# Performance work log

Hardware: AMD Instinct MI355X
Metric: run time of the kernel (lower is better)

Reference implementation:

```python
import jax, jax.numpy as jnp
import numpy as np

B, C, H, W = 8, 128, 64, 64

def setup_inputs() -> dict:
    key = jax.random.key(0)
    ks = jax.random.split(key, 8)
    s = 1.0 / np.sqrt(C)
    return {
        "x": jax.random.normal(ks[0], (B, C, H, W), dtype=jnp.float32),
        "dw_q": jax.random.normal(ks[1], (C,), dtype=jnp.float32) * s,
        "pw_q": jax.random.normal(ks[2], (C, C), dtype=jnp.float32) * s,
        "dw_k": jax.random.normal(ks[3], (C,), dtype=jnp.float32) * s,
        "pw_k": jax.random.normal(ks[4], (C, C), dtype=jnp.float32) * s,
        "dw_v": jax.random.normal(ks[5], (C,), dtype=jnp.float32) * s,
        "pw_v": jax.random.normal(ks[6], (C, C), dtype=jnp.float32) * s,
        "gamma": jnp.zeros((1,), dtype=jnp.float32) + 0.5,
    }

def _proj(x, dw, pw):
    # depthwise 1x1 (groups=C, no bias) == per-channel scale; then pointwise 1x1 conv (C_out=C)
    xs = x * dw[None, :, None, None]
    return jnp.einsum('oc,bchw->bohw', pw, xs)

def reference(x, dw_q, pw_q, dw_k, pw_k, dw_v, pw_v, gamma):
    b, c, h, w = x.shape
    n = h * w
    q = _proj(x, dw_q, pw_q).reshape(b, c, n)   # B,C,N
    k = _proj(x, dw_k, pw_k).reshape(b, c, n)
    v = _proj(x, dw_v, pw_v).reshape(b, c, n)
    # energy[b,n,m] = sum_c q[b,c,n] k[b,c,m]  (no scaling, as in source)
    energy = jnp.einsum('bcn,bcm->bnm', q, k)
    attn = jax.nn.softmax(energy, axis=-1)      # B,N,N
    # out[b,c,n] = sum_m v[b,c,m] attn[b,n,m]
    out = jnp.einsum('bcm,bnm->bcn', v, attn).reshape(b, c, h, w)
    return gamma[0] * out + x
```

## Files before the change

### kernel.cpp

```cpp
#include <hip/hip_runtime.h>
#include <hip/hip_bf16.h>


typedef __bf16 v8bf __attribute__((ext_vector_type(8)));
typedef float  v4f  __attribute__((ext_vector_type(4)));

#define B_ 8
#define C_ 128
#define N_ 4096

#define SWZ(R, COLS) ((R) * 160 + (((((COLS) >> 3) ^ (((R) >> 2) & 15))) << 3) + ((COLS) & 7))

static __device__ __forceinline__ unsigned short f2bf_rne(float f) {
    union { float f; unsigned u; } v; v.f = f;
    return (unsigned short)((v.u + 0x7fffu + ((v.u >> 16) & 1u)) >> 16);
}
static __device__ __forceinline__ unsigned fbits(float f) {
    union { float f; unsigned u; } v; v.f = f; return v.u;
}

__global__ __launch_bounds__(256, 2) void proj_kernel(
    const float* __restrict__ x,
    const float* __restrict__ dw_q, const float* __restrict__ pw_q,
    const float* __restrict__ dw_k, const float* __restrict__ pw_k,
    const float* __restrict__ dw_v, const float* __restrict__ pw_v,
    unsigned short* __restrict__ qf_ws, unsigned short* __restrict__ kt,
    unsigned short* __restrict__ vt)
{
    __shared__ unsigned short xT[128 * 160];
    __shared__ unsigned short Ws[128 * 160];

    const int bid = blockIdx.x;
    const int bb  = bid & 7;
    const int t   = (bid >> 3) & 31;
    const int pp  = bid >> 8;
    const int n0  = t * 128;
    const int tid = threadIdx.x;
    const int w    = tid >> 6;
    const int lane = tid & 63;
    const int quad = lane >> 4;
    const int l16  = lane & 15;

    #pragma unroll
    for (int k = 0; k < 16; ++k) {
        const int idx = tid + k * 256;
        const int c  = idx >> 5;
        const int nq = idx & 31;
        float4 f = *(const float4*)(x + ((size_t)(bb * C_ + c)) * N_ + n0 + nq * 4);
        xT[SWZ(nq * 4 + 0, c)] = f2bf_rne(f.x);
        xT[SWZ(nq * 4 + 1, c)] = f2bf_rne(f.y);
        xT[SWZ(nq * 4 + 2, c)] = f2bf_rne(f.z);
        xT[SWZ(nq * 4 + 3, c)] = f2bf_rne(f.w);
    }
    const float* pw = (pp == 0) ? pw_q : (pp == 1) ? pw_k : pw_v;
    const float* dw = (pp == 0) ? dw_q : (pp == 1) ? dw_k : dw_v;
    const float qs = (pp == 0) ? 1.4426950408889634f : 1.0f;
    #pragma unroll
    for (int k = 0; k < 16; ++k) {
        const int idx = tid + k * 256;
        const int o  = idx >> 5;
        const int c4 = (idx & 31) * 4;
        float4 p4 = *(const float4*)(pw + o * 128 + c4);
        float4 d4 = *(const float4*)(dw + c4);
        unsigned lo = (unsigned)f2bf_rne(p4.x * d4.x * qs) | ((unsigned)f2bf_rne(p4.y * d4.y * qs) << 16);
        unsigned hi = (unsigned)f2bf_rne(p4.z * d4.z * qs) | ((unsigned)f2bf_rne(p4.w * d4.w * qs) << 16);
        *(unsigned long long*)&Ws[SWZ(o, c4)] =
            (unsigned long long)lo | ((unsigned long long)hi << 32);
    }
    __syncthreads();

    const unsigned short* As = (pp < 2) ? xT : Ws;
    const unsigned short* Bs = (pp < 2) ? Ws : xT;

    v4f acc[2][8];
    #pragma unroll
    for (int i = 0; i < 2; ++i)
        #pragma unroll
        for (int j = 0; j < 8; ++j)
            acc[i][j] = (v4f){0.f, 0.f, 0.f, 0.f};

    #pragma unroll
    for (int kc = 0; kc < 4; ++kc) {
        v8bf av[2];
        #pragma unroll
        for (int i = 0; i < 2; ++i)
            av[i] = *(const v8bf*)&As[SWZ(w * 32 + i * 16 + l16, kc * 32 + quad * 8)];
        #pragma unroll
        for (int cb = 0; cb < 8; ++cb) {
            v8bf bv = *(const v8bf*)&Bs[SWZ(cb * 16 + l16, kc * 32 + quad * 8)];
            acc[0][cb] = __builtin_amdgcn_mfma_f32_16x16x32_bf16(av[0], bv, acc[0][cb], 0, 0, 0);
            acc[1][cb] = __builtin_amdgcn_mfma_f32_16x16x32_bf16(av[1], bv, acc[1][cb], 0, 0, 0);
        }
    }
    __syncthreads();

    unsigned short* sc = Ws;
    #pragma unroll
    for (int mi = 0; mi < 2; ++mi)
        #pragma unroll
        for (int cb = 0; cb < 8; ++cb)
            #pragma unroll
            for (int r = 0; r < 4; ++r)
                sc[SWZ(w * 32 + mi * 16 + quad * 4 + r, cb * 16 + l16)] =
                    f2bf_rne(acc[mi][cb][r]);
    __syncthreads();

    if (pp == 0) {
        unsigned short* dst = qf_ws + ((size_t)(bb * 64 + t * 2)) * 8192;
        #pragma unroll
        for (int p = 0; p < 8; ++p) {
            const int g     = p * 4 + w;
            const int strip = g >> 4, ni = (g >> 2) & 3, kc = g & 3;
            *(uint4*)(dst + ((size_t)g * 64 + lane) * 8) =
                *(const uint4*)&sc[SWZ(strip * 64 + ni * 16 + l16, kc * 32 + quad * 8)];
        }
    } else if (pp == 1) {
        unsigned short* dst = kt + ((size_t)(bb * 32 + t)) * 16384;
        #pragma unroll
        for (int p = 0; p < 8; ++p) {
            const int g  = p * 4 + w;
            const int mb = g >> 2, kc = g & 3;
            *(uint4*)(dst + ((size_t)g * 64 + lane) * 8) =
                *(const uint4*)&sc[SWZ(mb * 16 + l16, kc * 32 + quad * 8)];
        }
    } else {
        unsigned short* dst = vt + ((size_t)(bb * 32 + t)) * 16384;
        #pragma unroll
        for (int p = 0; p < 8; ++p) {
            const int d  = p * 256 + tid;
            const int cb = d >> 8, wq = (d >> 4) & 15, l = d & 15;
            *(uint4*)(dst + (size_t)d * 8) =
                *(const uint4*)&sc[SWZ(cb * 16 + l, wq * 8)];
        }
    }
}

#define MFMA(A, B, C) __builtin_amdgcn_mfma_f32_16x16x32_bf16(A, B, C, 0, 0, 0)
#define EXP2(X) __builtin_amdgcn_exp2f(X)
#define PKPERM(EH, EL) __builtin_amdgcn_perm(fbits(EH), fbits(EL), 0x07060302)

#define LOADK(KF, TILE) { \
    const unsigned short* kp_ = kbase + (size_t)(TILE) * 16384; \
    _Pragma("unroll") \
    for (int mi_ = 0; mi_ < 2; ++mi_) \
        _Pragma("unroll") \
        for (int kc_ = 0; kc_ < 4; ++kc_) \
            KF[mi_][kc_] = *(const v8bf*)(kp_ + (size_t)((mi_ * 4 + kc_) * 64) * 8); \
}

#define LOADV(TILE) { \
    const unsigned short* vp_ = vbase + (size_t)(TILE) * 16384; \
    _Pragma("unroll") \
    for (int cb_ = 0; cb_ < 8; ++cb_) \
        vf[cb_] = *(const v8bf*)(vp_ + (size_t)(cb_ * 256) * 8); \
}

#define MKPF(NI, PK0A, PK0B, PK1A, PK1B) { \
    unsigned sLo_ = (quad < 2) ? PK0A : PK1A; \
    unsigned sHi_ = (quad < 2) ? PK0B : PK1B; \
    union { unsigned u[4]; v8bf v; } pu_; \
    pu_.u[0] = (unsigned)__builtin_amdgcn_ds_bpermute(la, (int)sLo_); \
    pu_.u[1] = (unsigned)__builtin_amdgcn_ds_bpermute(la, (int)sHi_); \
    pu_.u[2] = (unsigned)__builtin_amdgcn_ds_bpermute(lb, (int)sLo_); \
    pu_.u[3] = (unsigned)__builtin_amdgcn_ds_bpermute(lb, (int)sHi_); \
    pf[NI] = pu_.v; \
}

#define SCOMP0(KF, SC) { \
    _Pragma("unroll") \
    for (int mi_ = 0; mi_ < 2; ++mi_) \
        _Pragma("unroll") \
        for (int ni_ = 0; ni_ < 2; ++ni_) { \
            v4f a_ = MFMA(KF[mi_][0], qf[ni_][0], Z4v); \
            _Pragma("unroll") \
            for (int kc_ = 1; kc_ < 4; ++kc_) \
                a_ = MFMA(KF[mi_][kc_], qf[ni_][kc_], a_); \
            SC[mi_][ni_] = a_; \
        } \
}

#define FUSED(SC_IN, KF, SC_OUT) { \
    float e0_, e1_, e2_, e3_; \
    unsigned pk00a_, pk00b_, pk10a_, pk10b_, pk01a_, pk01b_, pk11a_, pk11b_; \
    SC_OUT[0][0] = MFMA(KF[0][0], qf[0][0], Z4v); \
    SC_OUT[0][1] = MFMA(KF[0][0], qf[1][0], Z4v); \
    e0_ = EXP2(SC_IN[0][0][0]); e1_ = EXP2(SC_IN[0][0][1]); \
    e2_ = EXP2(SC_IN[0][0][2]); e3_ = EXP2(SC_IN[0][0][3]); \
    SC_OUT[0][0] = MFMA(KF[0][1], qf[0][1], SC_OUT[0][0]); \
    SC_OUT[0][1] = MFMA(KF[0][1], qf[1][1], SC_OUT[0][1]); \
    lpart[0] += (e0_ + e1_) + (e2_ + e3_); \
    pk00a_ = PKPERM(e1_, e0_); pk00b_ = PKPERM(e3_, e2_); \
    SC_OUT[0][0] = MFMA(KF[0][2], qf[0][2], SC_OUT[0][0]); \
    SC_OUT[0][1] = MFMA(KF[0][2], qf[1][2], SC_OUT[0][1]); \
    e0_ = EXP2(SC_IN[1][0][0]); e1_ = EXP2(SC_IN[1][0][1]); \
    e2_ = EXP2(SC_IN[1][0][2]); e3_ = EXP2(SC_IN[1][0][3]); \
    SC_OUT[0][0] = MFMA(KF[0][3], qf[0][3], SC_OUT[0][0]); \
    SC_OUT[0][1] = MFMA(KF[0][3], qf[1][3], SC_OUT[0][1]); \
    lpart[0] += (e0_ + e1_) + (e2_ + e3_); \
    pk10a_ = PKPERM(e1_, e0_); pk10b_ = PKPERM(e3_, e2_); \
    SC_OUT[1][0] = MFMA(KF[1][0], qf[0][0], Z4v); \
    SC_OUT[1][1] = MFMA(KF[1][0], qf[1][0], Z4v); \
    MKPF(0, pk00a_, pk00b_, pk10a_, pk10b_) \
    SC_OUT[1][0] = MFMA(KF[1][1], qf[0][1], SC_OUT[1][0]); \
    SC_OUT[1][1] = MFMA(KF[1][1], qf[1][1], SC_OUT[1][1]); \
    e0_ = EXP2(SC_IN[0][1][0]); e1_ = EXP2(SC_IN[0][1][1]); \
    e2_ = EXP2(SC_IN[0][1][2]); e3_ = EXP2(SC_IN[0][1][3]); \
    SC_OUT[1][0] = MFMA(KF[1][2], qf[0][2], SC_OUT[1][0]); \
    SC_OUT[1][1] = MFMA(KF[1][2], qf[1][2], SC_OUT[1][1]); \
    lpart[1] += (e0_ + e1_) + (e2_ + e3_); \
    pk01a_ = PKPERM(e1_, e0_); pk01b_ = PKPERM(e3_, e2_); \
    SC_OUT[1][0] = MFMA(KF[1][3], qf[0][3], SC_OUT[1][0]); \
    SC_OUT[1][1] = MFMA(KF[1][3], qf[1][3], SC_OUT[1][1]); \
    e0_ = EXP2(SC_IN[1][1][0]); e1_ = EXP2(SC_IN[1][1][1]); \
    e2_ = EXP2(SC_IN[1][1][2]); e3_ = EXP2(SC_IN[1][1][3]); \
    lpart[1] += (e0_ + e1_) + (e2_ + e3_); \
    pk11a_ = PKPERM(e1_, e0_); pk11b_ = PKPERM(e3_, e2_); \
    MKPF(1, pk01a_, pk01b_, pk11a_, pk11b_) \
}

#define PVOP { \
    _Pragma("unroll") \
    for (int ni_ = 0; ni_ < 2; ++ni_) \
        _Pragma("unroll") \
        for (int cb_ = 0; cb_ < 8; ++cb_) \
            oacc[cb_][ni_] = MFMA(vf[cb_], pf[ni_], oacc[cb_][ni_]); \
}

__global__ __launch_bounds__(256, 2) void attn_kernel(
    const unsigned short* __restrict__ qf_ws, const unsigned short* __restrict__ kt,
    const unsigned short* __restrict__ vt, const float* __restrict__ x,
    const float* __restrict__ gamma, float* __restrict__ out)
{
    __shared__ float red[32 * 132];
    __shared__ float l_s[4][32];

    const int bid = blockIdx.x;
    const int bb  = bid & 7;
    const int s   = bid >> 3;
    const int n0  = s * 32;
    const int tid = threadIdx.x;
    const int w    = tid >> 6;
    const int lane = tid & 63;
    const int quad = lane >> 4;
    const int l16  = lane & 15;

    v8bf qf[2][4];
    {
        const unsigned short* qb = qf_ws + ((size_t)(bb * 128 + s)) * 4096;
        #pragma unroll
        for (int ni = 0; ni < 2; ++ni)
            #pragma unroll
            for (int kc = 0; kc < 4; ++kc)
                qf[ni][kc] = *(const v8bf*)(qb + ((size_t)(ni * 4 + kc) * 64 + lane) * 8);
    }

    v4f oacc[8][2];
    #pragma unroll
    for (int i = 0; i < 8; ++i)
        #pragma unroll
        for (int j = 0; j < 2; ++j)
            oacc[i][j] = (v4f){0.f, 0.f, 0.f, 0.f};
    float lpart[2] = {0.f, 0.f};
    const v4f Z4v = {0.f, 0.f, 0.f, 0.f};

    const int la = ((((quad & 1) << 1) << 4) + l16) << 2;
    const int lb = la + 64;

    const unsigned short* kbase = kt + ((size_t)(bb * 32)) * 16384 + ((size_t)(w * 8) * 64 + lane) * 8;
    const unsigned short* vbase = vt + ((size_t)(bb * 32)) * 16384 + ((size_t)(w * 64 + lane)) * 8;

    v8bf kfA[2][4], kfB[2][4], vf[8];
    v4f sc0[2][2], sc1[2][2];
    v8bf pf[2];

    LOADK(kfA, 0)
    LOADV(0)
    LOADK(kfB, 1)
    SCOMP0(kfA, sc0)

    for (int it = 0; it < 32; it += 2) {
        LOADK(kfA, (it + 2) & 31)
        FUSED(sc0, kfB, sc1)
        PVOP
        LOADV((it + 1) & 31)
        LOADK(kfB, (it + 3) & 31)
        FUSED(sc1, kfA, sc0)
        PVOP
        LOADV((it + 2) & 31)
    }

    #pragma unroll
    for (int ni = 0; ni < 2; ++ni) {
        float r = lpart[ni];
        r += __shfl_xor(r, 16);
        r += __shfl_xor(r, 32);
        if (lane < 16) l_s[w][ni * 16 + lane] = r;
    }

    for (int rw = 0; rw < 4; ++rw) {
        if (w == rw) {
            #pragma unroll
            for (int cb = 0; cb < 8; ++cb)
                #pragma unroll
                for (int ni = 0; ni < 2; ++ni) {
                    float* p = &red[(ni * 16 + l16) * 132 + cb * 16 + quad * 4];
                    if (rw == 0) *(v4f*)p = oacc[cb][ni];
                    else {
                        v4f tv = *(const v4f*)p;
                        tv += oacc[cb][ni];
                        *(v4f*)p = tv;
                    }
                }
        }
        __syncthreads();
    }

    const float g = gamma[0];
    const int   n = tid & 31;
    const int  cg = tid >> 5;
    const float li = 1.0f / (((l_s[0][n] + l_s[1][n]) + (l_s[2][n] + l_s[3][n])));
    #pragma unroll
    for (int j = 0; j < 16; ++j) {
        const int c = cg * 16 + j;
        const size_t idx = ((size_t)(bb * C_ + c)) * N_ + n0 + n;
        out[idx] = g * red[n * 132 + c] * li + x[idx];
    }
}

extern "C" void kernel_launch(void* const* d_in, const int* in_sizes, int n_in,
                              void* d_out, int out_size, void* d_ws, size_t ws_size,
                              hipStream_t stream)
{
    (void)in_sizes; (void)n_in; (void)out_size; (void)ws_size;
    const float* x     = (const float*)d_in[0];
    const float* dw_q  = (const float*)d_in[1];
    const float* pw_q  = (const float*)d_in[2];
    const float* dw_k  = (const float*)d_in[3];
    const float* pw_k  = (const float*)d_in[4];
    const float* dw_v  = (const float*)d_in[5];
    const float* pw_v  = (const float*)d_in[6];
    const float* gamma = (const float*)d_in[7];
    float* out = (float*)d_out;

    unsigned short* qf_ws = (unsigned short*)d_ws;
    unsigned short* kt    = qf_ws + (size_t)B_ * N_ * C_;
    unsigned short* vt    = kt    + (size_t)B_ * N_ * C_;

    proj_kernel<<<dim3(768), dim3(256), 0, stream>>>(
        x, dw_q, pw_q, dw_k, pw_k, dw_v, pw_v, qf_ws, kt, vt);
    attn_kernel<<<dim3(1024), dim3(256), 0, stream>>>(
        qf_ws, kt, vt, x, gamma, out);
}
```

Measured before the change: 174.1 us.

## Switch attention Q/K/V and probabilities to FP8 MFMA

Projection outputs Q, K and V are now packed to FP8 (e4m3) in a new fragment layout, and the attention kernel uses 16x16x32 fp8 MFMA for both QK^T and PV. Softmax probabilities are packed to FP8 with cvt_pk_fp8, which halves the ds_bpermute traffic. The aim is to halve workspace bandwidth and register footprint and to use higher-throughput FP8 matrix ops. In exchange, the much lower precision of the scores and probabilities (no scaling is applied) risks accuracy failures, especially since the unscaled energies feed exp2.

```diff
diff --git a/kernel.cpp b/kernel.cpp
--- a/kernel.cpp
+++ b/kernel.cpp
@@ -4,6 +4,7 @@
 
 typedef __bf16 v8bf __attribute__((ext_vector_type(8)));
 typedef float  v4f  __attribute__((ext_vector_type(4)));
+typedef unsigned long long u64;
 
 #define B_ 8
 #define C_ 128
@@ -15,8 +16,19 @@
     union { float f; unsigned u; } v; v.f = f;
     return (unsigned short)((v.u + 0x7fffu + ((v.u >> 16) & 1u)) >> 16);
 }
-static __device__ __forceinline__ unsigned fbits(float f) {
-    union { float f; unsigned u; } v; v.f = f; return v.u;
+
+static __device__ __forceinline__ u64 bf8pack(uint4 s) {
+    float f[8];
+    #pragma unroll
+    for (int j = 0; j < 8; ++j) {
+        unsigned hs = (j & 1) ? ((&s.x)[j >> 1] >> 16) : ((&s.x)[j >> 1] & 0xffffu);
+        union { unsigned u; float f; } t; t.u = hs << 16; f[j] = t.f;
+    }
+    int lo = __builtin_amdgcn_cvt_pk_fp8_f32(f[0], f[1], 0, false);
+    lo     = __builtin_amdgcn_cvt_pk_fp8_f32(f[2], f[3], lo, true);
+    int hi = __builtin_amdgcn_cvt_pk_fp8_f32(f[4], f[5], 0, false);
+    hi     = __builtin_amdgcn_cvt_pk_fp8_f32(f[6], f[7], hi, true);
+    return (u64)(unsigned)lo | ((u64)(unsigned)hi << 32);
 }
 
 __global__ __launch_bounds__(256, 2) void proj_kernel(
@@ -24,8 +36,8 @@
     const float* __restrict__ dw_q, const float* __restrict__ pw_q,
     const float* __restrict__ dw_k, const float* __restrict__ pw_k,
     const float* __restrict__ dw_v, const float* __restrict__ pw_v,
-    unsigned short* __restrict__ qf_ws, unsigned short* __restrict__ kt,
-    unsigned short* __restrict__ vt)
+    unsigned char* __restrict__ qf8, unsigned char* __restrict__ kt8,
+    unsigned char* __restrict__ vt8)
 {
     __shared__ unsigned short xT[128 * 160];
     __shared__ unsigned short Ws[128 * 160];
@@ -106,64 +118,80 @@
     __syncthreads();
 
     if (pp == 0) {
-        unsigned short* dst = qf_ws + ((size_t)(bb * 64 + t * 2)) * 8192;
+        unsigned char* dst = qf8 + (size_t)bb * 524288;
         #pragma unroll
         for (int p = 0; p < 8; ++p) {
             const int g     = p * 4 + w;
             const int strip = g >> 4, ni = (g >> 2) & 3, kc = g & 3;
-            *(uint4*)(dst + ((size_t)g * 64 + lane) * 8) =
-                *(const uint4*)&sc[SWZ(strip * 64 + ni * 16 + l16, kc * 32 + quad * 8)];
+            uint4 sv = *(const uint4*)&sc[SWZ(strip * 64 + ni * 16 + l16, kc * 32 + quad * 8)];
+            *(u64*)(dst + (size_t)(t * 4 + strip * 2 + (ni >> 1)) * 4096
+                        + ((ni & 1) * 2 + (kc >> 1)) * 1024 + lane * 16 + (kc & 1) * 8)
+                = bf8pack(sv);
         }
     } else if (pp == 1) {
-        unsigned short* dst = kt + ((size_t)(bb * 32 + t)) * 16384;
+        unsigned char* dst = kt8 + (size_t)(bb * 32 + t) * 16384;
         #pragma unroll
         for (int p = 0; p < 8; ++p) {
             const int g  = p * 4 + w;
             const int mb = g >> 2, kc = g & 3;
-            *(uint4*)(dst + ((size_t)g * 64 + lane) * 8) =
-                *(const uint4*)&sc[SWZ(mb * 16 + l16, kc * 32 + quad * 8)];
+            uint4 sv = *(const uint4*)&sc[SWZ(mb * 16 + l16, kc * 32 + quad * 8)];
+            *(u64*)(dst + (mb * 2 + (kc >> 1)) * 1024 + lane * 16 + (kc & 1) * 8)
+                = bf8pack(sv);
         }
     } else {
-        unsigned short* dst = vt + ((size_t)(bb * 32 + t)) * 16384;
+        unsigned char* dst = vt8 + (size_t)(bb * 32 + t) * 16384;
         #pragma unroll
         for (int p = 0; p < 8; ++p) {
-            const int d  = p * 256 + tid;
-            const int cb = d >> 8, wq = (d >> 4) & 15, l = d & 15;
-            *(uint4*)(dst + (size_t)d * 8) =
-                *(const uint4*)&sc[SWZ(cb * 16 + l, wq * 8)];
-        }
-    }
-}
-
-#define MFMA(A, B, C) __builtin_amdgcn_mfma_f32_16x16x32_bf16(A, B, C, 0, 0, 0)
+            const int d   = p * 256 + tid;
+            const int cb  = d >> 8;
+            const int wqm = (d >> 6) & 3;
+            const int q16 = (d >> 4) & 15;
+            const int l   = d & 15;
+            const int lnS = d & 63;
+            uint4 sv = *(const uint4*)&sc[SWZ(cb * 16 + l, q16 * 8)];
+            *(u64*)(dst + ((cb >> 1) * 4 + wqm) * 1024 + lnS * 16 + (cb & 1) * 8)
+                = bf8pack(sv);
+        }
+    }
+}
+
+#define MFMA8(A, B, C) __builtin_amdgcn_mfma_f32_16x16x32_fp8_fp8((long)(A), (long)(B), C, 0, 0, 0)
 #define EXP2(X) __builtin_amdgcn_exp2f(X)
-#define PKPERM(EH, EL) __builtin_amdgcn_perm(fbits(EH), fbits(EL), 0x07060302)
+#define PK8(E0, E1, E2, E3, W) { \
+    W = __builtin_amdgcn_cvt_pk_fp8_f32(E0, E1, 0, false); \
+    W = __builtin_amdgcn_cvt_pk_fp8_f32(E2, E3, W, true); \
+}
+
+#define SPLIT16(U4, LO, HI) { \
+    LO = (u64)(U4).x | ((u64)(U4).y << 32); \
+    HI = (u64)(U4).z | ((u64)(U4).w << 32); \
+}
 
 #define LOADK(KF, TILE) { \
-    const unsigned short* kp_ = kbase + (size_t)(TILE) * 16384; \
+    const unsigned char* kp_ = kbase + (size_t)(TILE) * 16384; \
     _Pragma("unroll") \
     for (int mi_ = 0; mi_ < 2; ++mi_) \
         _Pragma("unroll") \
-        for (int kc_ = 0; kc_ < 4; ++kc_) \
-            KF[mi_][kc_] = *(const v8bf*)(kp_ + (size_t)((mi_ * 4 + kc_) * 64) * 8); \
+        for (int kcp_ = 0; kcp_ < 2; ++kcp_) { \
+            uint4 u_ = *(const uint4*)(kp_ + (mi_ * 2 + kcp_) * 1024); \
+            SPLIT16(u_, KF[mi_][kcp_ * 2], KF[mi_][kcp_ * 2 + 1]) \
+        } \
 }
 
 #define LOADV(TILE) { \
-    const unsigned short* vp_ = vbase + (size_t)(TILE) * 16384; \
+    const unsigned char* vp_ = vbase + (size_t)(TILE) * 16384; \
     _Pragma("unroll") \
-    for (int cb_ = 0; cb_ < 8; ++cb_) \
-        vf[cb_] = *(const v8bf*)(vp_ + (size_t)(cb_ * 256) * 8); \
-}
-
-#define MKPF(NI, PK0A, PK0B, PK1A, PK1B) { \
-    unsigned sLo_ = (quad < 2) ? PK0A : PK1A; \
-    unsigned sHi_ = (quad < 2) ? PK0B : PK1B; \
-    union { unsigned u[4]; v8bf v; } pu_; \
-    pu_.u[0] = (unsigned)__builtin_amdgcn_ds_bpermute(la, (int)sLo_); \
-    pu_.u[1] = (unsigned)__builtin_amdgcn_ds_bpermute(la, (int)sHi_); \
-    pu_.u[2] = (unsigned)__builtin_amdgcn_ds_bpermute(lb, (int)sLo_); \
-    pu_.u[3] = (unsigned)__builtin_amdgcn_ds_bpermute(lb, (int)sHi_); \
-    pf[NI] = pu_.v; \
+    for (int cbp_ = 0; cbp_ < 4; ++cbp_) { \
+        uint4 u_ = *(const uint4*)(vp_ + cbp_ * 4096); \
+        SPLIT16(u_, vf[cbp_ * 2], vf[cbp_ * 2 + 1]) \
+    } \
+}
+
+#define MKPF8(NI, PK0, PK1) { \
+    int s_ = (quad < 2) ? PK0 : PK1; \
+    u64 lo_ = (unsigned)__builtin_amdgcn_ds_bpermute(la, s_); \
+    u64 hi_ = (unsigned)__builtin_amdgcn_ds_bpermute(lb, s_); \
+    pf[NI] = lo_ | (hi_ << 32); \
 }
 
 #define SCOMP0(KF, SC) { \
@@ -171,51 +199,51 @@
     for (int mi_ = 0; mi_ < 2; ++mi_) \
         _Pragma("unroll") \
         for (int ni_ = 0; ni_ < 2; ++ni_) { \
-            v4f a_ = MFMA(KF[mi_][0], qf[ni_][0], Z4v); \
+            v4f a_ = MFMA8(KF[mi_][0], qf[ni_][0], Z4v); \
             _Pragma("unroll") \
             for (int kc_ = 1; kc_ < 4; ++kc_) \
-                a_ = MFMA(KF[mi_][kc_], qf[ni_][kc_], a_); \
+                a_ = MFMA8(KF[mi_][kc_], qf[ni_][kc_], a_); \
             SC[mi_][ni_] = a_; \
         } \
 }
 
 #define FUSED(SC_IN, KF, SC_OUT) { \
     float e0_, e1_, e2_, e3_; \
-    unsigned pk00a_, pk00b_, pk10a_, pk10b_, pk01a_, pk01b_, pk11a_, pk11b_; \
-    SC_OUT[0][0] = MFMA(KF[0][0], qf[0][0], Z4v); \
-    SC_OUT[0][1] = MFMA(KF[0][0], qf[1][0], Z4v); \
+    int pk00_, pk10_, pk01_, pk11_; \
+    SC_OUT[0][0] = MFMA8(KF[0][0], qf[0][0], Z4v); \
+    SC_OUT[0][1] = MFMA8(KF[0][0], qf[1][0], Z4v); \
     e0_ = EXP2(SC_IN[0][0][0]); e1_ = EXP2(SC_IN[0][0][1]); \
     e2_ = EXP2(SC_IN[0][0][2]); e3_ = EXP2(SC_IN[0][0][3]); \
-    SC_OUT[0][0] = MFMA(KF[0][1], qf[0][1], SC_OUT[0][0]); \
-    SC_OUT[0][1] = MFMA(KF[0][1], qf[1][1], SC_OUT[0][1]); \
+    SC_OUT[0][0] = MFMA8(KF[0][1], qf[0][1], SC_OUT[0][0]); \
+    SC_OUT[0][1] = MFMA8(KF[0][1], qf[1][1], SC_OUT[0][1]); \
     lpart[0] += (e0_ + e1_) + (e2_ + e3_); \
-    pk00a_ = PKPERM(e1_, e0_); pk00b_ = PKPERM(e3_, e2_); \
-    SC_OUT[0][0] = MFMA(KF[0][2], qf[0][2], SC_OUT[0][0]); \
-    SC_OUT[0][1] = MFMA(KF[0][2], qf[1][2], SC_OUT[0][1]); \
+    PK8(e0_, e1_, e2_, e3_, pk00_) \
+    SC_OUT[0][0] = MFMA8(KF[0][2], qf[0][2], SC_OUT[0][0]); \
+    SC_OUT[0][1] = MFMA8(KF[0][2], qf[1][2], SC_OUT[0][1]); \
     e0_ = EXP2(SC_IN[1][0][0]); e1_ = EXP2(SC_IN[1][0][1]); \
     e2_ = EXP2(SC_IN[1][0][2]); e3_ = EXP2(SC_IN[1][0][3]); \
-    SC_OUT[0][0] = MFMA(KF[0][3], qf[0][3], SC_OUT[0][0]); \
-    SC_OUT[0][1] = MFMA(KF[0][3], qf[1][3], SC_OUT[0][1]); \
+    SC_OUT[0][0] = MFMA8(KF[0][3], qf[0][3], SC_OUT[0][0]); \
+    SC_OUT[0][1] = MFMA8(KF[0][3], qf[1][3], SC_OUT[0][1]); \
     lpart[0] += (e0_ + e1_) + (e2_ + e3_); \
-    pk10a_ = PKPERM(e1_, e0_); pk10b_ = PKPERM(e3_, e2_); \
-    SC_OUT[1][0] = MFMA(KF[1][0], qf[0][0], Z4v); \
-    SC_OUT[1][1] = MFMA(KF[1][0], qf[1][0], Z4v); \
-    MKPF(0, pk00a_, pk00b_, pk10a_, pk10b_) \
-    SC_OUT[1][0] = MFMA(KF[1][1], qf[0][1], SC_OUT[1][0]); \
-    SC_OUT[1][1] = MFMA(KF[1][1], qf[1][1], SC_OUT[1][1]); \
+    PK8(e0_, e1_, e2_, e3_, pk10_) \
+    SC_OUT[1][0] = MFMA8(KF[1][0], qf[0][0], Z4v); \
+    SC_OUT[1][1] = MFMA8(KF[1][0], qf[1][0], Z4v); \
+    MKPF8(0, pk00_, pk10_) \
+    SC_OUT[1][0] = MFMA8(KF[1][1], qf[0][1], SC_OUT[1][0]); \
+    SC_OUT[1][1] = MFMA8(KF[1][1], qf[1][1], SC_OUT[1][1]); \
     e0_ = EXP2(SC_IN[0][1][0]); e1_ = EXP2(SC_IN[0][1][1]); \
     e2_ = EXP2(SC_IN[0][1][2]); e3_ = EXP2(SC_IN[0][1][3]); \
-    SC_OUT[1][0] = MFMA(KF[1][2], qf[0][2], SC_OUT[1][0]); \
-    SC_OUT[1][1] = MFMA(KF[1][2], qf[1][2], SC_OUT[1][1]); \
+    SC_OUT[1][0] = MFMA8(KF[1][2], qf[0][2], SC_OUT[1][0]); \
+    SC_OUT[1][1] = MFMA8(KF[1][2], qf[1][2], SC_OUT[1][1]); \
     lpart[1] += (e0_ + e1_) + (e2_ + e3_); \
-    pk01a_ = PKPERM(e1_, e0_); pk01b_ = PKPERM(e3_, e2_); \
-    SC_OUT[1][0] = MFMA(KF[1][3], qf[0][3], SC_OUT[1][0]); \
-    SC_OUT[1][1] = MFMA(KF[1][3], qf[1][3], SC_OUT[1][1]); \
+    PK8(e0_, e1_, e2_, e3_, pk01_) \
+    SC_OUT[1][0] = MFMA8(KF[1][3], qf[0][3], SC_OUT[1][0]); \
+    SC_OUT[1][1] = MFMA8(KF[1][3], qf[1][3], SC_OUT[1][1]); \
     e0_ = EXP2(SC_IN[1][1][0]); e1_ = EXP2(SC_IN[1][1][1]); \
     e2_ = EXP2(SC_IN[1][1][2]); e3_ = EXP2(SC_IN[1][1][3]); \
     lpart[1] += (e0_ + e1_) + (e2_ + e3_); \
-    pk11a_ = PKPERM(e1_, e0_); pk11b_ = PKPERM(e3_, e2_); \
-    MKPF(1, pk01a_, pk01b_, pk11a_, pk11b_) \
+    PK8(e0_, e1_, e2_, e3_, pk11_) \
+    MKPF8(1, pk01_, pk11_) \
 }
 
 #define PVOP { \
@@ -223,12 +251,12 @@
     for (int ni_ = 0; ni_ < 2; ++ni_) \
         _Pragma("unroll") \
         for (int cb_ = 0; cb_ < 8; ++cb_) \
-            oacc[cb_][ni_] = MFMA(vf[cb_], pf[ni_], oacc[cb_][ni_]); \
+            oacc[cb_][ni_] = MFMA8(vf[cb_], pf[ni_], oacc[cb_][ni_]); \
 }
 
 __global__ __launch_bounds__(256, 2) void attn_kernel(
-    const unsigned short* __restrict__ qf_ws, const unsigned short* __restrict__ kt,
-    const unsigned short* __restrict__ vt, const float* __restrict__ x,
+    const unsigned char* __restrict__ qf8, const unsigned char* __restrict__ kt8,
+    const unsigned char* __restrict__ vt8, const float* __restrict__ x,
     const float* __restrict__ gamma, float* __restrict__ out)
 {
     __shared__ float red[32 * 132];
@@ -244,14 +272,16 @@
     const int quad = lane >> 4;
     const int l16  = lane & 15;
 
-    v8bf qf[2][4];
+    u64 qf[2][4];
     {
-        const unsigned short* qb = qf_ws + ((size_t)(bb * 128 + s)) * 4096;
+        const unsigned char* qb = qf8 + (size_t)(bb * 128 + s) * 4096 + lane * 16;
         #pragma unroll
         for (int ni = 0; ni < 2; ++ni)
             #pragma unroll
-            for (int kc = 0; kc < 4; ++kc)
-                qf[ni][kc] = *(const v8bf*)(qb + ((size_t)(ni * 4 + kc) * 64 + lane) * 8);
+            for (int kcp = 0; kcp < 2; ++kcp) {
+                uint4 u = *(const uint4*)(qb + (ni * 2 + kcp) * 1024);
+                SPLIT16(u, qf[ni][kcp * 2], qf[ni][kcp * 2 + 1])
+            }
     }
 
     v4f oacc[8][2];
@@ -266,12 +296,11 @@
     const int la = ((((quad & 1) << 1) << 4) + l16) << 2;
     const int lb = la + 64;
 
-    const unsigned short* kbase = kt + ((size_t)(bb * 32)) * 16384 + ((size_t)(w * 8) * 64 + lane) * 8;
-    const unsigned short* vbase = vt + ((size_t)(bb * 32)) * 16384 + ((size_t)(w * 64 + lane)) * 8;
-
-    v8bf kfA[2][4], kfB[2][4], vf[8];
+    const unsigned char* kbase = kt8 + (size_t)(bb * 32) * 16384 + w * 4096 + lane * 16;
+    const unsigned char* vbase = vt8 + (size_t)(bb * 32) * 16384 + w * 1024 + lane * 16;
+
+    u64 kfA[2][4], kfB[2][4], vf[8], pf[2];
     v4f sc0[2][2], sc1[2][2];
-    v8bf pf[2];
 
     LOADK(kfA, 0)
     LOADV(0)
@@ -342,12 +371,12 @@
     const float* gamma = (const float*)d_in[7];
     float* out = (float*)d_out;
 
-    unsigned short* qf_ws = (unsigned short*)d_ws;
-    unsigned short* kt    = qf_ws + (size_t)B_ * N_ * C_;
-    unsigned short* vt    = kt    + (size_t)B_ * N_ * C_;
+    unsigned char* qf8 = (unsigned char*)d_ws;
+    unsigned char* kt8 = qf8 + (size_t)B_ * N_ * C_ / 2 * 2;
+    unsigned char* vt8 = kt8 + (size_t)B_ * N_ * C_;
 
     proj_kernel<<<dim3(768), dim3(256), 0, stream>>>(
-        x, dw_q, pw_q, dw_k, pw_k, dw_v, pw_v, qf_ws, kt, vt);
+        x, dw_q, pw_q, dw_k, pw_k, dw_v, pw_v, qf8, kt8, vt8);
     attn_kernel<<<dim3(1024), dim3(256), 0, stream>>>(
-        qf_ws, kt, vt, x, gamma, out);
-}
+        qf8, kt8, vt8, x, gamma, out);
+}
```

New measurement: 154.1 us. 1.13x faster.
